# Kernel optimization log

Measured on AMD Instinct MI355X. Metric: run time of the kernel, lower is better.

## Reference

```python
import jax, jax.numpy as jnp
import numpy as np
from jax import lax


def _edt(mask):
    """Exact Euclidean distance transform: for boolean mask [B,H,W], return the
    distance from each True pixel to the nearest False pixel (0 on False pixels).
    Two-phase separable algorithm:
      phase 1: 1D distance along axis H (rows) via forward/backward scans.
      phase 2: D2[i,j] = min_j' ( g[i,j']^2 + (j-j')^2 ) along axis W.
    """
    B, H, W = mask.shape
    BIG = jnp.float32(H + W)  # cap: larger than any in-image distance
    mT = jnp.transpose(mask, (1, 0, 2))  # [H,B,W] for scanning over rows

    def step(carry, m_row):
        d = jnp.where(m_row, jnp.minimum(carry + 1.0, BIG), 0.0)
        return d, d

    init = jnp.full((B, W), BIG, dtype=jnp.float32)
    _, fwd = lax.scan(step, init, mT)          # dist to nearest False above
    _, bwd = lax.scan(step, init, mT[::-1])    # dist to nearest False below
    g = jnp.minimum(fwd, bwd[::-1])            # [H,B,W] exact 1D vertical distance
    g2 = g * g

    j = jnp.arange(W, dtype=jnp.float32)
    sq = (j[:, None] - j[None, :]) ** 2        # [W(j), W(j')]
    # D2[h,b,j] = min_j' g2[h,b,j'] + (j-j')^2   (intermediate [H,B,W,W])
    D2 = jnp.min(g2[..., None, :] + sq, axis=-1)
    return jnp.sqrt(D2).transpose(1, 0, 2)     # [B,H,W]


def _dt(z):
    """Faithful port of the torch `dt`: fg-EDT + bg-EDT, zero if no foreground."""
    fg = z > 0.5
    f_dist = _edt(fg)        # distance from foreground pixels to background
    b_dist = _edt(~fg)       # distance from background pixels to foreground
    has_fg = jnp.any(fg, axis=(1, 2))[:, None, None]
    return jnp.where(has_fg, f_dist + b_dist, 0.0)


def setup_inputs() -> dict:
    key = jax.random.key(0)
    kx, ky = jax.random.split(key)
    x = jax.random.uniform(kx, (8, 256, 256), dtype=jnp.float32)
    y = jax.random.uniform(ky, (8, 256, 256), dtype=jnp.float32)
    return {"x": x, "y": y}


def reference(x, y):
    # distance transforms are computed on detached tensors in the original
    dt_x = lax.stop_gradient(_dt(x))
    dt_y = lax.stop_gradient(_dt(y))
    err = (x - y) ** 2
    dist = dt_x ** 2 + dt_y ** 2
    return jnp.mean(err * dist)
```

## Files before the change

kernel.cpp:

```cpp
#include <hip/hip_runtime.h>

#define BB 8
#define HH 256
#define WW 256
#define BHW (BB*HH*WW)
#define BIGV 512.0f


__global__ __launch_bounds__(256) void edt_vert(const float* __restrict__ x,
                                                const float* __restrict__ y,
                                                unsigned short* __restrict__ gdist,
                                                int* __restrict__ blkflag,
                                                float* __restrict__ out) {
    __shared__ float Cf[2][16][16];
    __shared__ float Cb[2][16][16];
    __shared__ int sAny;

    int blk = blockIdx.x;
    int tileIdx = blk & 15;
    int b  = (blk >> 4) & 7;
    int ip = blk >> 7;
    int t = threadIdx.x;
    int c = t & 15, s = t >> 4;

    if (t == 0) sAny = 0;
    if (blk == 0 && t == 0) out[0] = 0.0f;

    const float* src = (ip ? y : x) + (size_t)b*HH*WW + tileIdx*16 + c;

    unsigned m = 0;
    const float* p = src + (size_t)(s*16)*WW;
    #pragma unroll
    for (int i = 0; i < 16; ++i) {
        if (p[(size_t)i*WW] > 0.5f) m |= (1u << i);
    }

    unsigned invm = (~m) & 0xFFFFu;
    Cf[0][s][c] = invm ? (float)(15 - (31 - __clz((int)invm))) : 1e9f;
    Cb[0][s][c] = invm ? (float)(__ffs((int)invm) - 1)          : 1e9f;
    Cf[1][s][c] = m    ? (float)(15 - (31 - __clz((int)m)))     : 1e9f;
    Cb[1][s][c] = m    ? (float)(__ffs((int)m) - 1)             : 1e9f;
    __syncthreads();
    if (m) sAny = 1;

    float e0 = BIGV, e1 = BIGV;
    #pragma unroll
    for (int sp = 0; sp < 15; ++sp) {
        float c0 = Cf[0][sp][c], c1 = Cf[1][sp][c];
        bool act = sp < s;
        e0 = act ? fminf(fminf(e0 + 16.0f, BIGV), c0) : e0;
        e1 = act ? fminf(fminf(e1 + 16.0f, BIGV), c1) : e1;
    }
    float f0 = BIGV, f1 = BIGV;
    #pragma unroll
    for (int sp = 15; sp >= 1; --sp) {
        float c0 = Cb[0][sp][c], c1 = Cb[1][sp][c];
        bool act = sp > s;
        f0 = act ? fminf(fminf(f0 + 16.0f, BIGV), c0) : f0;
        f1 = act ? fminf(fminf(f1 + 16.0f, BIGV), c1) : f1;
    }

    float b0v[16], b1v[16];
    float d0 = f0, d1 = f1;
    #pragma unroll
    for (int i = 15; i >= 0; --i) {
        bool bit = (m >> i) & 1u;
        d0 = !bit ? 0.0f : fminf(d0 + 1.0f, BIGV);
        d1 =  bit ? 0.0f : fminf(d1 + 1.0f, BIGV);
        b0v[i] = d0; b1v[i] = d1;
    }
    size_t base = (size_t)(ip*BB + b)*HH*WW + tileIdx*16 + c;
    d0 = e0; d1 = e1;
    #pragma unroll
    for (int i = 0; i < 16; ++i) {
        bool bit = (m >> i) & 1u;
        d0 = !bit ? 0.0f : fminf(d0 + 1.0f, BIGV);
        d1 =  bit ? 0.0f : fminf(d1 + 1.0f, BIGV);
        float g0 = fminf(d0, b0v[i]);
        float g1 = fminf(d1, b1v[i]);
        float gs = bit ? g0 : g1;
        gdist[base + (size_t)(s*16 + i)*WW] = (unsigned short)(int)gs;
    }

    __syncthreads();
    if (t == 0) blkflag[blk] = sAny;
}

__global__ __launch_bounds__(1024) void row_band(const float* __restrict__ x,
                                                 const float* __restrict__ y,
                                                 const unsigned short* __restrict__ gdist,
                                                 const int* __restrict__ blkflag,
                                                 float* __restrict__ out) {
    __shared__ float sp[4][4][768];
    __shared__ float wsum[16];
    __shared__ float sF[2];
    int blk = blockIdx.x;
    int b    = blk >> 4;
    int band = blk & 15;
    int t = threadIdx.x;
    int j  = t & 255;
    int rs = t >> 8;

    if (t < 64) {
        int v = 0;
        if (t < 32) v = blkflag[((t < 16) ? 0 : 128) + b * 16 + (t & 15)];
        unsigned long long ball = __ballot(v != 0);
        if (t == 0) {
            sF[0] = (ball & 0xFFFFull) ? 1.0f : 0.0f;
            sF[1] = ((ball >> 16) & 0xFFFFull) ? 1.0f : 0.0f;
        }
    }

    float acc = 0.0f;
    #pragma unroll
    for (int iter = 0; iter < 4; ++iter) {
        int row = band * 16 + rs + iter * 4;
        size_t rowoff = ((size_t)b * HH + row) * WW;

        float xv = x[rowoff + j];
        float yv = y[rowoff + j];
        int gx = gdist[rowoff + j];
        int gy = gdist[(size_t)BHW + rowoff + j];
        bool mx = xv > 0.5f;
        bool my = yv > 0.5f;
        int gx2 = gx * gx, gy2 = gy * gy;
        float v0 = (float)(mx ? gx2 : 0);
        float v1 = (float)(mx ? 0 : gx2);
        float v2 = (float)(my ? gy2 : 0);
        float v3 = (float)(my ? 0 : gy2);

        sp[rs][0][j] = 1e9f; sp[rs][1][j] = 1e9f; sp[rs][2][j] = 1e9f; sp[rs][3][j] = 1e9f;
        sp[rs][0][j+512] = 1e9f; sp[rs][1][j+512] = 1e9f; sp[rs][2][j+512] = 1e9f; sp[rs][3][j+512] = 1e9f;
        sp[rs][0][j+256] = v0; sp[rs][1][j+256] = v1; sp[rs][2][j+256] = v2; sp[rs][3][j+256] = v3;
        __syncthreads();

        float b0 = v0, b1 = v1, b2 = v2, b3 = v3;
        for (int dl = 1; dl < 256; ++dl) {
            float d2 = (float)(dl * dl);
            float bmax = fmaxf(fmaxf(b0, b1), fmaxf(b2, b3));
            if (!__any(d2 < bmax)) break;
            int l = j + 256 - dl, r = j + 256 + dl;
            b0 = fminf(b0, fminf(d2 + sp[rs][0][l], d2 + sp[rs][0][r]));
            b1 = fminf(b1, fminf(d2 + sp[rs][1][l], d2 + sp[rs][1][r]));
            b2 = fminf(b2, fminf(d2 + sp[rs][2][l], d2 + sp[rs][2][r]));
            b3 = fminf(b3, fminf(d2 + sp[rs][3][l], d2 + sp[rs][3][r]));
        }

        float dtx = sF[0] != 0.0f ? (sqrtf(b0) + sqrtf(b1)) : 0.0f;
        float dty = sF[1] != 0.0f ? (sqrtf(b2) + sqrtf(b3)) : 0.0f;
        float e = xv - yv;
        acc += e * e * (dtx * dtx + dty * dty);
        __syncthreads();
    }

    for (int off = 32; off; off >>= 1) acc += __shfl_down(acc, off, 64);
    int wid = t >> 6, lane = t & 63;
    if (lane == 0) wsum[wid] = acc;
    __syncthreads();
    if (t == 0) {
        float s = 0.0f;
        #pragma unroll
        for (int i = 0; i < 16; ++i) s += wsum[i];
        atomicAdd(out, s * (1.0f / (float)BHW));
    }
}

extern "C" void kernel_launch(void* const* d_in, const int* in_sizes, int n_in,
                              void* d_out, int out_size, void* d_ws, size_t ws_size,
                              hipStream_t stream) {
    const float* x = (const float*)d_in[0];
    const float* y = (const float*)d_in[1];
    float* out = (float*)d_out;

    char* ws = (char*)d_ws;
    unsigned short* gdist = (unsigned short*)ws;
    int* blkflag = (int*)(ws + (size_t)2 * BHW * sizeof(unsigned short));

    edt_vert<<<256, 256, 0, stream>>>(x, y, gdist, blkflag, out);
    row_band<<<128, 1024, 0, stream>>>(x, y, gdist, blkflag, out);
}
```

Measured before the change: 17.65 us.

## Split work into more blocks and replace atomic accumulation with a reduce kernel

The vertical pass now uses 8-row by 8-column tiles across 512 blocks instead of 16x16 tiles across 256 blocks. The row pass launches 1024 blocks of 512 threads, each handling two rows once instead of looping over four, and writes per-row partial sums. A third single-block kernel sums the partials and writes the mean, replacing the atomicAdd into a zeroed output. The intent is to fill more compute units and shorten the serial per-block work, at the cost of an extra kernel launch and a longer scan over 32 segments in the vertical pass.

New measurement: 18.48 us. 4.7% more time.

```diff
diff --git a/kernel.cpp b/kernel.cpp
--- a/kernel.cpp
+++ b/kernel.cpp
@@ -10,159 +10,160 @@
 __global__ __launch_bounds__(256) void edt_vert(const float* __restrict__ x,
                                                 const float* __restrict__ y,
                                                 unsigned short* __restrict__ gdist,
-                                                int* __restrict__ blkflag,
-                                                float* __restrict__ out) {
-    __shared__ float Cf[2][16][16];
-    __shared__ float Cb[2][16][16];
+                                                int* __restrict__ blkflag) {
+    __shared__ float Cf[2][32][8];
+    __shared__ float Cb[2][32][8];
     __shared__ int sAny;
 
     int blk = blockIdx.x;
-    int tileIdx = blk & 15;
-    int b  = (blk >> 4) & 7;
-    int ip = blk >> 7;
+    int tileIdx = blk & 31;
+    int b  = (blk >> 5) & 7;
+    int ip = blk >> 8;
     int t = threadIdx.x;
-    int c = t & 15, s = t >> 4;
+    int c = t & 7, s = t >> 3;
 
     if (t == 0) sAny = 0;
-    if (blk == 0 && t == 0) out[0] = 0.0f;
 
-    const float* src = (ip ? y : x) + (size_t)b*HH*WW + tileIdx*16 + c;
+    const float* src = (ip ? y : x) + (size_t)b*HH*WW + tileIdx*8 + c;
 
     unsigned m = 0;
-    const float* p = src + (size_t)(s*16)*WW;
+    const float* p = src + (size_t)(s*8)*WW;
     #pragma unroll
-    for (int i = 0; i < 16; ++i) {
+    for (int i = 0; i < 8; ++i) {
         if (p[(size_t)i*WW] > 0.5f) m |= (1u << i);
     }
 
-    unsigned invm = (~m) & 0xFFFFu;
-    Cf[0][s][c] = invm ? (float)(15 - (31 - __clz((int)invm))) : 1e9f;
-    Cb[0][s][c] = invm ? (float)(__ffs((int)invm) - 1)          : 1e9f;
-    Cf[1][s][c] = m    ? (float)(15 - (31 - __clz((int)m)))     : 1e9f;
-    Cb[1][s][c] = m    ? (float)(__ffs((int)m) - 1)             : 1e9f;
+    unsigned invm = (~m) & 0xFFu;
+    Cf[0][s][c] = invm ? (float)(7 - (31 - __clz((int)invm))) : 1e9f;
+    Cb[0][s][c] = invm ? (float)(__ffs((int)invm) - 1)         : 1e9f;
+    Cf[1][s][c] = m    ? (float)(7 - (31 - __clz((int)m)))     : 1e9f;
+    Cb[1][s][c] = m    ? (float)(__ffs((int)m) - 1)            : 1e9f;
     __syncthreads();
     if (m) sAny = 1;
 
     float e0 = BIGV, e1 = BIGV;
     #pragma unroll
-    for (int sp = 0; sp < 15; ++sp) {
+    for (int sp = 0; sp < 31; ++sp) {
         float c0 = Cf[0][sp][c], c1 = Cf[1][sp][c];
         bool act = sp < s;
-        e0 = act ? fminf(fminf(e0 + 16.0f, BIGV), c0) : e0;
-        e1 = act ? fminf(fminf(e1 + 16.0f, BIGV), c1) : e1;
+        e0 = act ? fminf(fminf(e0 + 8.0f, BIGV), c0) : e0;
+        e1 = act ? fminf(fminf(e1 + 8.0f, BIGV), c1) : e1;
     }
     float f0 = BIGV, f1 = BIGV;
     #pragma unroll
-    for (int sp = 15; sp >= 1; --sp) {
+    for (int sp = 31; sp >= 1; --sp) {
         float c0 = Cb[0][sp][c], c1 = Cb[1][sp][c];
         bool act = sp > s;
-        f0 = act ? fminf(fminf(f0 + 16.0f, BIGV), c0) : f0;
-        f1 = act ? fminf(fminf(f1 + 16.0f, BIGV), c1) : f1;
+        f0 = act ? fminf(fminf(f0 + 8.0f, BIGV), c0) : f0;
+        f1 = act ? fminf(fminf(f1 + 8.0f, BIGV), c1) : f1;
     }
 
-    float b0v[16], b1v[16];
+    float b0v[8], b1v[8];
     float d0 = f0, d1 = f1;
     #pragma unroll
-    for (int i = 15; i >= 0; --i) {
+    for (int i = 7; i >= 0; --i) {
         bool bit = (m >> i) & 1u;
         d0 = !bit ? 0.0f : fminf(d0 + 1.0f, BIGV);
         d1 =  bit ? 0.0f : fminf(d1 + 1.0f, BIGV);
         b0v[i] = d0; b1v[i] = d1;
     }
-    size_t base = (size_t)(ip*BB + b)*HH*WW + tileIdx*16 + c;
+    size_t base = (size_t)(ip*BB + b)*HH*WW + tileIdx*8 + c;
     d0 = e0; d1 = e1;
     #pragma unroll
-    for (int i = 0; i < 16; ++i) {
+    for (int i = 0; i < 8; ++i) {
         bool bit = (m >> i) & 1u;
         d0 = !bit ? 0.0f : fminf(d0 + 1.0f, BIGV);
         d1 =  bit ? 0.0f : fminf(d1 + 1.0f, BIGV);
         float g0 = fminf(d0, b0v[i]);
         float g1 = fminf(d1, b1v[i]);
         float gs = bit ? g0 : g1;
-        gdist[base + (size_t)(s*16 + i)*WW] = (unsigned short)(int)gs;
+        gdist[base + (size_t)(s*8 + i)*WW] = (unsigned short)(int)gs;
     }
 
     __syncthreads();
     if (t == 0) blkflag[blk] = sAny;
 }
 
-__global__ __launch_bounds__(1024) void row_band(const float* __restrict__ x,
-                                                 const float* __restrict__ y,
-                                                 const unsigned short* __restrict__ gdist,
-                                                 const int* __restrict__ blkflag,
-                                                 float* __restrict__ out) {
-    __shared__ float sp[4][4][768];
-    __shared__ float wsum[16];
+__global__ __launch_bounds__(512) void row_pass(const float* __restrict__ x,
+                                                const float* __restrict__ y,
+                                                const unsigned short* __restrict__ gdist,
+                                                const int* __restrict__ blkflag,
+                                                float* __restrict__ partials) {
+    __shared__ float sp[2][4][768];
+    __shared__ float wsum[8];
     __shared__ float sF[2];
     int blk = blockIdx.x;
-    int b    = blk >> 4;
-    int band = blk & 15;
+    int b  = blk >> 7;
+    int hh = blk & 127;
     int t = threadIdx.x;
     int j  = t & 255;
     int rs = t >> 8;
+    int h  = hh*2 + rs;
+    size_t rowoff = ((size_t)b * HH + h) * WW;
+
+    float xv = x[rowoff + j];
+    float yv = y[rowoff + j];
+    int gx = gdist[rowoff + j];
+    int gy = gdist[(size_t)BHW + rowoff + j];
+    bool mx = xv > 0.5f;
+    bool my = yv > 0.5f;
+    int gx2 = gx * gx, gy2 = gy * gy;
+    float v0 = (float)(mx ? gx2 : 0);
+    float v1 = (float)(mx ? 0 : gx2);
+    float v2 = (float)(my ? gy2 : 0);
+    float v3 = (float)(my ? 0 : gy2);
+
+    sp[rs][0][j] = 1e9f; sp[rs][1][j] = 1e9f; sp[rs][2][j] = 1e9f; sp[rs][3][j] = 1e9f;
+    sp[rs][0][j+512] = 1e9f; sp[rs][1][j+512] = 1e9f; sp[rs][2][j+512] = 1e9f; sp[rs][3][j+512] = 1e9f;
+    sp[rs][0][j+256] = v0; sp[rs][1][j+256] = v1; sp[rs][2][j+256] = v2; sp[rs][3][j+256] = v3;
 
     if (t < 64) {
-        int v = 0;
-        if (t < 32) v = blkflag[((t < 16) ? 0 : 128) + b * 16 + (t & 15)];
+        int v = (t < 32) ? blkflag[b * 32 + t] : blkflag[256 + b * 32 + (t - 32)];
         unsigned long long ball = __ballot(v != 0);
         if (t == 0) {
-            sF[0] = (ball & 0xFFFFull) ? 1.0f : 0.0f;
-            sF[1] = ((ball >> 16) & 0xFFFFull) ? 1.0f : 0.0f;
+            sF[0] = (ball & 0xFFFFFFFFull) ? 1.0f : 0.0f;
+            sF[1] = (ball >> 32)           ? 1.0f : 0.0f;
         }
     }
+    __syncthreads();
 
-    float acc = 0.0f;
-    #pragma unroll
-    for (int iter = 0; iter < 4; ++iter) {
-        int row = band * 16 + rs + iter * 4;
-        size_t rowoff = ((size_t)b * HH + row) * WW;
-
-        float xv = x[rowoff + j];
-        float yv = y[rowoff + j];
-        int gx = gdist[rowoff + j];
-        int gy = gdist[(size_t)BHW + rowoff + j];
-        bool mx = xv > 0.5f;
-        bool my = yv > 0.5f;
-        int gx2 = gx * gx, gy2 = gy * gy;
-        float v0 = (float)(mx ? gx2 : 0);
-        float v1 = (float)(mx ? 0 : gx2);
-        float v2 = (float)(my ? gy2 : 0);
-        float v3 = (float)(my ? 0 : gy2);
-
-        sp[rs][0][j] = 1e9f; sp[rs][1][j] = 1e9f; sp[rs][2][j] = 1e9f; sp[rs][3][j] = 1e9f;
-        sp[rs][0][j+512] = 1e9f; sp[rs][1][j+512] = 1e9f; sp[rs][2][j+512] = 1e9f; sp[rs][3][j+512] = 1e9f;
-        sp[rs][0][j+256] = v0; sp[rs][1][j+256] = v1; sp[rs][2][j+256] = v2; sp[rs][3][j+256] = v3;
-        __syncthreads();
-
-        float b0 = v0, b1 = v1, b2 = v2, b3 = v3;
-        for (int dl = 1; dl < 256; ++dl) {
-            float d2 = (float)(dl * dl);
-            float bmax = fmaxf(fmaxf(b0, b1), fmaxf(b2, b3));
-            if (!__any(d2 < bmax)) break;
-            int l = j + 256 - dl, r = j + 256 + dl;
-            b0 = fminf(b0, fminf(d2 + sp[rs][0][l], d2 + sp[rs][0][r]));
-            b1 = fminf(b1, fminf(d2 + sp[rs][1][l], d2 + sp[rs][1][r]));
-            b2 = fminf(b2, fminf(d2 + sp[rs][2][l], d2 + sp[rs][2][r]));
-            b3 = fminf(b3, fminf(d2 + sp[rs][3][l], d2 + sp[rs][3][r]));
-        }
-
-        float dtx = sF[0] != 0.0f ? (sqrtf(b0) + sqrtf(b1)) : 0.0f;
-        float dty = sF[1] != 0.0f ? (sqrtf(b2) + sqrtf(b3)) : 0.0f;
-        float e = xv - yv;
-        acc += e * e * (dtx * dtx + dty * dty);
-        __syncthreads();
+    float b0 = v0, b1 = v1, b2 = v2, b3 = v3;
+    for (int dl = 1; dl < 256; ++dl) {
+        float d2 = (float)(dl * dl);
+        float bmax = fmaxf(fmaxf(b0, b1), fmaxf(b2, b3));
+        if (!__any(d2 < bmax)) break;
+        int l = j + 256 - dl, r = j + 256 + dl;
+        b0 = fminf(b0, fminf(d2 + sp[rs][0][l], d2 + sp[rs][0][r]));
+        b1 = fminf(b1, fminf(d2 + sp[rs][1][l], d2 + sp[rs][1][r]));
+        b2 = fminf(b2, fminf(d2 + sp[rs][2][l], d2 + sp[rs][2][r]));
+        b3 = fminf(b3, fminf(d2 + sp[rs][3][l], d2 + sp[rs][3][r]));
     }
 
-    for (int off = 32; off; off >>= 1) acc += __shfl_down(acc, off, 64);
-    int wid = t >> 6, lane = t & 63;
-    if (lane == 0) wsum[wid] = acc;
+    float dtx = sF[0] != 0.0f ? (sqrtf(b0) + sqrtf(b1)) : 0.0f;
+    float dty = sF[1] != 0.0f ? (sqrtf(b2) + sqrtf(b3)) : 0.0f;
+    float e = xv - yv;
+    float val = e * e * (dtx * dtx + dty * dty);
+
+    for (int off = 32; off; off >>= 1) val += __shfl_down(val, off, 64);
+    if ((t & 63) == 0) wsum[t >> 6] = val;
     __syncthreads();
     if (t == 0) {
-        float s = 0.0f;
-        #pragma unroll
-        for (int i = 0; i < 16; ++i) s += wsum[i];
-        atomicAdd(out, s * (1.0f / (float)BHW));
+        partials[(size_t)b * HH + hh*2 + 0] = wsum[0] + wsum[1] + wsum[2] + wsum[3];
+        partials[(size_t)b * HH + hh*2 + 1] = wsum[4] + wsum[5] + wsum[6] + wsum[7];
     }
+}
+
+__global__ __launch_bounds__(256) void final_reduce(const float* __restrict__ partials,
+                                                    float* __restrict__ out) {
+    __shared__ float wsum[4];
+    int j = threadIdx.x;
+    float s = 0.0f;
+    #pragma unroll
+    for (int i = 0; i < 8; ++i) s += partials[i * 256 + j];
+    for (int off = 32; off; off >>= 1) s += __shfl_down(s, off, 64);
+    if ((j & 63) == 0) wsum[j >> 6] = s;
+    __syncthreads();
+    if (j == 0) out[0] = (wsum[0] + wsum[1] + wsum[2] + wsum[3]) * (1.0f / (float)BHW);
 }
 
 extern "C" void kernel_launch(void* const* d_in, const int* in_sizes, int n_in,
@@ -175,7 +176,9 @@
     char* ws = (char*)d_ws;
     unsigned short* gdist = (unsigned short*)ws;
     int* blkflag = (int*)(ws + (size_t)2 * BHW * sizeof(unsigned short));
+    float* partials = (float*)(ws + (size_t)2 * BHW * sizeof(unsigned short) + 512 * sizeof(int));
 
-    edt_vert<<<256, 256, 0, stream>>>(x, y, gdist, blkflag, out);
-    row_band<<<128, 1024, 0, stream>>>(x, y, gdist, blkflag, out);
+    edt_vert<<<512, 256, 0, stream>>>(x, y, gdist, blkflag);
+    row_pass<<<1024, 512, 0, stream>>>(x, y, gdist, blkflag, partials);
+    final_reduce<<<1, 256, 0, stream>>>(partials, out);
 }
```
